# Kernel tuning notes

Measured on AMD Instinct MI355X. Metric: run time of the kernel, lower is better.

The kernel has to match this reference:

```python
import jax, jax.numpy as jnp
import numpy as np

POS_THR = 0.5      # ROI_POSITIVE_THR
NEG_THR = 0.1      # ROI_NEGATIVE_THR
N_SAMPLES = 256    # ROI_SAMPLES
FG_RATIO = 0.25    # ROI_SAMPLE_RATIO
L1W = 1.0          # RPN.L1WEIGHT_INTERSECTION
NUM_FG = int(N_SAMPLES * FG_RATIO)


def _make_boxes(kxy, kwh, shape):
    # valid [x1,y1,x2,y2] boxes in an ~800px image
    xy = jax.random.uniform(kxy, shape[:-1] + (2,)) * 800.0
    wh = jax.random.uniform(kwh, shape[:-1] + (2,)) * 200.0 + 1.0
    return jnp.concatenate([xy, xy + wh], axis=-1)


def setup_inputs() -> dict:
    key = jax.random.key(0)
    k1, k2, k3, k4 = jax.random.split(key, 4)
    proposals = _make_boxes(k1, k2, (16, 16384, 4))  # [B, N, 4]
    gt_boxes = _make_boxes(k3, k4, (16, 128, 4))     # [B, G, 4]
    return {"proposals": proposals, "gt_boxes": gt_boxes}


def _centrehw(b):
    # [x1,y1,x2,y2] -> [cx,cy,w,h]
    x1, y1, x2, y2 = b[..., 0], b[..., 1], b[..., 2], b[..., 3]
    return jnp.stack([(x1 + x2) * 0.5, (y1 + y2) * 0.5, x2 - x1, y2 - y1], axis=-1)


def _targets(gt_c, roi_c):
    dx = (gt_c[..., 0] - roi_c[..., 0]) / roi_c[..., 2]
    dy = (gt_c[..., 1] - roi_c[..., 1]) / roi_c[..., 3]
    dw = jnp.log(gt_c[..., 2] / roi_c[..., 2])
    dh = jnp.log(gt_c[..., 3] / roi_c[..., 3])
    return jnp.stack([dx, dy, dw, dh], axis=-1)


def _iou(prop, gt):
    # prop [B,N,4], gt [B,G,4] -> IoU [B,N,G]
    p = prop[:, :, None, :]
    g = gt[:, None, :, :]
    ix1 = jnp.maximum(p[..., 0], g[..., 0])
    iy1 = jnp.maximum(p[..., 1], g[..., 1])
    ix2 = jnp.minimum(p[..., 2], g[..., 2])
    iy2 = jnp.minimum(p[..., 3], g[..., 3])
    inter = jnp.clip(ix2 - ix1, 0.0) * jnp.clip(iy2 - iy1, 0.0)
    ap = (p[..., 2] - p[..., 0]) * (p[..., 3] - p[..., 1])
    ag = (g[..., 2] - g[..., 0]) * (g[..., 3] - g[..., 1])
    return inter / jnp.maximum(ap + ag - inter, 1e-8)


def _forward(proposals, gt_boxes):
    B, N, _ = proposals.shape
    iou = _iou(proposals, gt_boxes)                       # [B,N,G]
    max_iou = iou.max(axis=-1)                            # [B,N]
    argmax_gt = iou.argmax(axis=-1).astype(jnp.int32)     # [B,N]
    # classify: 1=fg, 0=bg, -1=ignore
    labels = jnp.where(max_iou >= POS_THR, 1,
                       jnp.where(max_iou < NEG_THR, 0, -1)).astype(jnp.int32)
    # randsample: keep <= NUM_FG positives (random), fill rest with negatives.
    r = jax.random.uniform(jax.random.key(1), (B, N))
    pos = labels == 1
    r_pos = jnp.where(pos, r, -1.0)
    order = jnp.argsort(-r_pos, axis=1)
    ranks = jnp.argsort(order, axis=1)                    # rank among positives by r
    pos_sel = pos & (ranks < NUM_FG)
    prio = jnp.where(pos_sel, 3.0 + r,
                     jnp.where(labels == 0, 2.0 + r,
                               jnp.where(pos, 1.0 + r, r)))
    _, idx = jax.lax.top_k(prio, N_SAMPLES)               # [B,S] sampled proposal ids
    batch_labels = jnp.maximum(jnp.take_along_axis(labels, idx, axis=1), 0)  # [B,S]
    roi_batch = jnp.take_along_axis(proposals, idx[..., None], axis=1)       # [B,S,4]
    sel_gt = jnp.take_along_axis(argmax_gt, idx, axis=1)                     # [B,S]
    gt_batch = jnp.take_along_axis(gt_boxes, sel_gt[..., None], axis=1)      # [B,S,4]
    bbox_targets = _targets(_centrehw(gt_batch), _centrehw(roi_batch))       # [B,S,4]
    in_w = jnp.where((batch_labels == 1)[..., None], L1W, 0.0)
    in_w = jnp.broadcast_to(in_w, bbox_targets.shape)
    out_w = (in_w > 0).astype(jnp.float32)
    return roi_batch, batch_labels, bbox_targets, in_w, out_w


def reference(proposals, gt_boxes):
    return _forward(proposals, gt_boxes)
```

## Files before the change

kernel.cpp:

```cpp
#include <hip/hip_runtime.h>
#include <stdint.h>

#define BATCH 16
#define NPROP 16384
#define NGT   128
#define NSAMP 256
#define NFG   64
#define GCAP  512
#define LCAP  8192
#define CSTR  32

typedef unsigned long long ull;

__device__ __forceinline__ void thr_block(uint32_t c0, uint32_t c1,
                                          uint32_t* o0, uint32_t* o1) {
    const uint32_t k0 = 0u, k1 = 1u, ks2 = 0x1BD11BDBu;
    uint32_t x0 = c0 + k0, x1 = c1 + k1;
#define RND(d) { x0 += x1; x1 = (x1 << d) | (x1 >> (32 - d)); x1 ^= x0; }
    RND(13) RND(15) RND(26) RND(6)   x0 += k1;  x1 += ks2 + 1u;
    RND(17) RND(29) RND(16) RND(24)  x0 += ks2; x1 += k0 + 2u;
    RND(13) RND(15) RND(26) RND(6)   x0 += k0;  x1 += k1 + 3u;
    RND(17) RND(29) RND(16) RND(24)  x0 += k1;  x1 += ks2 + 4u;
    RND(13) RND(15) RND(26) RND(6)   x0 += ks2; x1 += k0 + 5u;
#undef RND
    *o0 = x0; *o1 = x1;
}

__device__ __forceinline__ uint32_t thr_part_xor(uint32_t f) {
    uint32_t a, b; thr_block(0u, f, &a, &b);
    return a ^ b;
}

__global__ void k_zero(uint32_t* c) {
    if (threadIdx.x < BATCH * CSTR) c[threadIdx.x] = 0u;
}

__global__ void __launch_bounds__(256) k_compute(
    const float* __restrict__ props, const float* __restrict__ gts,
    ull* __restrict__ lists, uint32_t* __restrict__ cnts)
{
#pragma clang fp contract(off)
    const int b = blockIdx.y;
    const int tid = threadIdx.x;
    const int half = tid & 1;
    const int n = blockIdx.x * 128 + (tid >> 1);
    __shared__ float2 sA[130];
    __shared__ float2 sB[130];
    __shared__ float  sag[130];
    __shared__ uint32_t wcF[4], wcB[4], wcP[4];
    __shared__ uint32_t sEF[4], sEB[4], sBaseF, sBaseB;
    if (tid < NGT) {
        float4 g = ((const float4*)gts)[(size_t)b * NGT + tid];
        int idx = (tid < 64) ? tid : tid + 1;
        sA[idx] = make_float2(g.x, g.y);
        sB[idx] = make_float2(g.z, g.w);
        sag[idx] = (g.z - g.x) * (g.w - g.y);
    }
    __syncthreads();
    const float4 pb = ((const float4*)props)[(size_t)b * NPROP + n];
    const float ap = (pb.z - pb.x) * (pb.w - pb.y);
    float best = -1.0f; int bg = 0;
    const int base  = half ? 65 : 0;
    const int gbias = half ? 64 : 0;
    #pragma unroll 4
    for (int i = 0; i < 64; ++i) {
        const float2 a = sA[base + i];
        const float2 c = sB[base + i];
        float w  = fmaxf(fminf(pb.z, c.x) - fmaxf(pb.x, a.x), 0.0f);
        float hh = fmaxf(fminf(pb.w, c.y) - fmaxf(pb.y, a.y), 0.0f);
        float inter = w * hh;
        float un = fmaxf(ap + sag[base + i] - inter, 1e-8f);
        float iou = inter / un;
        if (iou > best) { best = iou; bg = gbias + i; }
    }
    float ob = __shfl_xor(best, 1);
    int  obg = __shfl_xor(bg, 1);
    if (half == 0 && ob > best) { best = ob; bg = obg; }

    uint32_t lab = (best >= 0.5f) ? 2u : ((best < 0.1f) ? 1u : 0u);
    const uint32_t f = (uint32_t)b * NPROP + (uint32_t)n;
    uint32_t mant = thr_part_xor(f) >> 9;
    ull entry = ((ull)(lab == 2u) << 44) | ((ull)mant << 21)
              | ((ull)(16383u - (uint32_t)n) << 7) | (ull)(uint32_t)bg;

    const bool isEven = (half == 0);
    bool front = isEven && (lab != 0u);
    bool back  = isEven && (lab == 0u);
    bool ispos = isEven && (lab == 2u);
    ull mF = __ballot(front), mB = __ballot(back), mP = __ballot(ispos);
    const int w = tid >> 6;
    const uint32_t lane = (uint32_t)tid & 63u;
    if (lane == 0) {
        wcF[w] = (uint32_t)__popcll(mF);
        wcB[w] = (uint32_t)__popcll(mB);
        wcP[w] = (uint32_t)__popcll(mP);
    }
    __syncthreads();
    if (tid == 0) {
        uint32_t eF = 0, eB = 0, tP = 0;
        #pragma unroll
        for (int i = 0; i < 4; i++) {
            sEF[i] = eF; eF += wcF[i];
            sEB[i] = eB; eB += wcB[i];
            tP += wcP[i];
        }
        sBaseF = eF ? atomicAdd(&cnts[b * CSTR + 0], eF) : 0u;
        sBaseB = eB ? atomicAdd(&cnts[b * CSTR + 1], eB) : 0u;
        if (tP) atomicAdd(&cnts[b * CSTR + 2], tP);
    }
    __syncthreads();
    ull lt = lane ? (~0ull >> (64u - lane)) : 0ull;
    ull* Lb = lists + (size_t)b * NPROP;
    if (front) Lb[sBaseF + sEF[w] + (uint32_t)__popcll(mF & lt)] = entry;
    if (back)  Lb[16383u - (sBaseB + sEB[w] + (uint32_t)__popcll(mB & lt))] = entry;
}

__global__ void __launch_bounds__(1024) k_select(
    const float* __restrict__ props, const float* __restrict__ gts,
    const ull* __restrict__ lists, const uint32_t* __restrict__ cnts,
    float* __restrict__ out)
{
#pragma clang fp contract(off)
    const int b = blockIdx.x;
    const int tid = threadIdx.x;
    __shared__ ull      sf[LCAP];
    __shared__ uint32_t hist[2048];
    __shared__ ull      gat[GCAP];
    __shared__ ull      selk[NSAMP];
    __shared__ uint32_t sela[NSAMP];
    __shared__ uint32_t sh_dig, sh_k, sh_cnt_in, gcnt, selc;
    __shared__ ull sh_thr;

    const ull* Lb = lists + (size_t)b * NPROP;
    const uint32_t npn  = cnts[b * CSTR + 0];
    const uint32_t nig  = cnts[b * CSTR + 1];
    const uint32_t npos = cnts[b * CSTR + 2];
    const bool inLDS = (npn <= LCAP);
    if (inLDS) for (uint32_t j = tid; j < npn; j += 1024) sf[j] = Lb[j];
    if (tid == 0) selc = 0;
    __syncthreads();

    auto getF = [&](uint32_t j) -> ull { return inLDS ? sf[j] : Lb[j]; };
    auto keyA_of = [&](ull e) -> ull {
        return (((e >> 21) & 0x7FFFFFull) << 14) | ((e >> 7) & 0x3FFFull);
    };

    auto locate = [&](uint32_t k) {
        if (tid < 64) {
            const uint32_t lane = (uint32_t)tid;
            uint32_t cs = 0;
            if (lane < 32) {
                const uint32_t base = lane * 64u;
                #pragma unroll 8
                for (uint32_t i = 0; i < 64; i++) cs += hist[base + i];
            }
            uint32_t s = cs;
            #pragma unroll
            for (int off = 1; off < 32; off <<= 1) {
                uint32_t t = __shfl_down(s, off);
                if (lane + off < 32) s += t;
            }
            uint32_t sExcl = s - cs;
            bool cond = (lane < 32) && (sExcl < k) && (k <= s);
            ull ball = __ballot(cond);
            uint32_t cstar = (uint32_t)(__ffsll((unsigned long long)ball) - 1);
            uint32_t kc = (uint32_t)__shfl((int)(k - sExcl), (int)cstar);
            uint32_t val = hist[cstar * 64u + lane];
            uint32_t fi = val;
            #pragma unroll
            for (int off = 1; off < 64; off <<= 1) {
                uint32_t t = __shfl_down(fi, off);
                if (lane + off < 64) fi += t;
            }
            uint32_t fExcl = fi - val;
            bool cond2 = (fExcl < kc) && (kc <= fi);
            ull ball2 = __ballot(cond2);
            uint32_t bstar = (uint32_t)(__ffsll((unsigned long long)ball2) - 1);
            if (lane == bstar) {
                sh_dig = cstar * 64u + lane;
                sh_k = kc - fExcl;
                sh_cnt_in = val;
            }
        }
    };

    auto radix = [&](auto&& kf, uint32_t m, uint32_t k, int shift) -> ull {
        ull prefix = 0, mask = 0;
        for (;;) {
            hist[tid] = 0; hist[tid + 1024] = 0;
            __syncthreads();
            for (uint32_t j = tid; j < m; j += 1024) {
                bool e; ull key = kf(j, e);
                if (e && ((key ^ prefix) & mask) == 0)
                    atomicAdd(&hist[(uint32_t)(key >> shift) & 2047u], 1u);
            }
            __syncthreads();
            locate(k);
            __syncthreads();
            uint32_t dig = sh_dig, kk = sh_k, cnt = sh_cnt_in;
            prefix |= ((ull)dig) << shift;
            mask   |= 2047ull << shift;
            if (cnt <= GCAP || shift == 0) {
                if (tid == 0) gcnt = 0;
                __syncthreads();
                for (uint32_t j = tid; j < m; j += 1024) {
                    bool e; ull key = kf(j, e);
                    if (e && ((key ^ prefix) & mask) == 0) {
                        uint32_t s = atomicAdd(&gcnt, 1u);
                        if (s < GCAP) gat[s] = key;
                    }
                }
                __syncthreads();
                uint32_t gc = (gcnt < GCAP) ? gcnt : GCAP;
                if (tid < (int)gc) {
                    ull x = gat[tid];
                    uint32_t r = 0;
                    for (uint32_t j = 0; j < gc; j++) r += (gat[j] > x);
                    if (r == kk - 1) sh_thr = x;
                }
                __syncthreads();
                return sh_thr;
            } else {
                k = kk;
                shift = (shift >= 11) ? shift - 11 : 0;
                __syncthreads();
            }
        }
    };

    ull thrA = 0;
    if (npos > NFG) {
        thrA = radix([&](uint32_t j, bool& e) -> ull {
            ull ent = getF(j);
            e = ((ent >> 44) & 1ull) != 0;
            return keyA_of(ent);
        }, npn, NFG, 26);
    }

    auto keyB_of = [&](ull ent) -> ull {
        uint32_t mant = (uint32_t)((ent >> 21) & 0x7FFFFFull);
        uint32_t invn = (uint32_t)((ent >> 7) & 0x3FFFull);
        float r = __uint_as_float(0x3F800000u | mant) - 1.0f;
        uint32_t cls;
        if ((ent >> 44) & 1ull) cls = (keyA_of(ent) >= thrA) ? 3u : 1u;
        else cls = 2u;
        float prio = (float)cls + r;
        return (((ull)__float_as_uint(prio)) << 14) | (ull)invn;
    };
    auto key0_of = [&](ull ent) -> ull {
        uint32_t mant = (uint32_t)((ent >> 21) & 0x7FFFFFull);
        uint32_t invn = (uint32_t)((ent >> 7) & 0x3FFFull);
        float r = __uint_as_float(0x3F800000u | mant) - 1.0f;
        float prio = 0.0f + r;
        return (((ull)__float_as_uint(prio)) << 14) | (ull)invn;
    };

    ull thrB = 0, thr0 = 0;
    uint32_t needIgn = 0;
    if (npn >= NSAMP) {
        thrB = radix([&](uint32_t j, bool& e) -> ull { e = true; return keyB_of(getF(j)); },
                     npn, NSAMP, 34);
    } else {
        needIgn = NSAMP - npn;
        thr0 = radix([&](uint32_t j, bool& e) -> ull { e = true; return key0_of(Lb[16383u - j]); },
                     nig, needIgn, 34);
    }
    __syncthreads();

    for (uint32_t j = tid; j < npn; j += 1024) {
        ull ent = getF(j);
        ull key = keyB_of(ent);
        if (npn < NSAMP || key >= thrB) {
            uint32_t s = atomicAdd(&selc, 1u);
            if (s < NSAMP) {
                selk[s] = key;
                sela[s] = ((uint32_t)((ent >> 44) & 1ull) << 7) | (uint32_t)(ent & 0x7Full);
            }
        }
    }
    if (needIgn) {
        for (uint32_t j = tid; j < nig; j += 1024) {
            ull ent = Lb[16383u - j];
            ull key = key0_of(ent);
            if (key >= thr0) {
                uint32_t s = atomicAdd(&selc, 1u);
                if (s < NSAMP) {
                    selk[s] = key;
                    sela[s] = (uint32_t)(ent & 0x7Full);
                }
            }
        }
    }
    __syncthreads();

    if (tid < NSAMP) {
        ull x = selk[tid];
        uint32_t r = 0;
        for (int j = 0; j < NSAMP; j++) r += (selk[j] > x);
        uint32_t n = 16383u - (uint32_t)(x & 0x3FFFull);
        uint32_t aux = sela[tid];
        uint32_t bg = aux & 0x7Fu;
        const int isfg = (int)((aux >> 7) & 1u);
        const float4 pb = ((const float4*)props)[(size_t)b * NPROP + n];
        const float4 gb = ((const float4*)gts)[(size_t)b * NGT + bg];
        const size_t O_ROI = 0;
        const size_t O_LBL = (size_t)BATCH * NSAMP * 4;
        const size_t O_TGT = O_LBL + (size_t)BATCH * NSAMP;
        const size_t O_INW = O_TGT + (size_t)BATCH * NSAMP * 4;
        const size_t O_OUW = O_INW + (size_t)BATCH * NSAMP * 4;
        const size_t row = (size_t)b * NSAMP + r;
        out[O_ROI + row * 4 + 0] = pb.x;
        out[O_ROI + row * 4 + 1] = pb.y;
        out[O_ROI + row * 4 + 2] = pb.z;
        out[O_ROI + row * 4 + 3] = pb.w;
        out[O_LBL + row] = isfg ? 1.0f : 0.0f;
        float rw  = pb.z - pb.x, rh = pb.w - pb.y;
        float gw  = gb.z - gb.x, gh = gb.w - gb.y;
        out[O_TGT + row * 4 + 0] = ((gb.x + gb.z) * 0.5f - (pb.x + pb.z) * 0.5f) / rw;
        out[O_TGT + row * 4 + 1] = ((gb.y + gb.w) * 0.5f - (pb.y + pb.w) * 0.5f) / rh;
        out[O_TGT + row * 4 + 2] = logf(gw / rw);
        out[O_TGT + row * 4 + 3] = logf(gh / rh);
        float wv = isfg ? 1.0f : 0.0f;
        for (int c = 0; c < 4; c++) {
            out[O_INW + row * 4 + c] = wv;
            out[O_OUW + row * 4 + c] = wv;
        }
    }
}

extern "C" void kernel_launch(void* const* d_in, const int* in_sizes, int n_in,
                              void* d_out, int out_size, void* d_ws, size_t ws_size,
                              hipStream_t stream) {
    (void)in_sizes; (void)n_in; (void)out_size; (void)ws_size;
    const float* props = (const float*)d_in[0];
    const float* gts   = (const float*)d_in[1];
    ull* lists = (ull*)d_ws;
    uint32_t* cnts = (uint32_t*)((char*)d_ws + (size_t)BATCH * NPROP * 8);
    float* out = (float*)d_out;

    k_zero<<<1, BATCH * CSTR, 0, stream>>>(cnts);
    dim3 gridA(NPROP / 128, BATCH);
    k_compute<<<gridA, 256, 0, stream>>>(props, gts, lists, cnts);
    k_select<<<BATCH, 1024, 0, stream>>>(props, gts, lists, cnts, out);
}
```

Before: 103.7 us.

## Bucket proposals into pos/high-neg/low-neg/ignore lists to shrink select radix work

The compute kernel now writes each proposal into one of four per-batch lists: positives, negatives with high random mantissa, negatives with low mantissa, and ignored. The select kernel uses the per-bucket counts to work out which priority class holds the cutoff and runs the radix threshold search only over that bucket, often just the high-negative list. Small lists go through a direct rank-count path instead of histogram passes. Counters are padded to separate cache lines. The costs are four times the workspace, an extra ballot and atomic per block, and reliance on the NEGT split putting enough negatives in the high bucket.

After: 96.23 us. 1.08x faster.

```diff
diff --git a/kernel.cpp b/kernel.cpp
--- a/kernel.cpp
+++ b/kernel.cpp
@@ -7,8 +7,8 @@
 #define NSAMP 256
 #define NFG   64
 #define GCAP  512
-#define LCAP  8192
-#define CSTR  32
+#define CSTR  128
+#define NEGT  0x780002u
 
 typedef unsigned long long ull;
 
@@ -32,7 +32,7 @@
 }
 
 __global__ void k_zero(uint32_t* c) {
-    if (threadIdx.x < BATCH * CSTR) c[threadIdx.x] = 0u;
+    for (int i = threadIdx.x; i < BATCH * CSTR; i += 1024) c[i] = 0u;
 }
 
 __global__ void __launch_bounds__(256) k_compute(
@@ -47,8 +47,9 @@
     __shared__ float2 sA[130];
     __shared__ float2 sB[130];
     __shared__ float  sag[130];
-    __shared__ uint32_t wcF[4], wcB[4], wcP[4];
-    __shared__ uint32_t sEF[4], sEB[4], sBaseF, sBaseB;
+    __shared__ uint32_t wc[4][4];
+    __shared__ uint32_t we[4][4];
+    __shared__ uint32_t sBase[4];
     if (tid < NGT) {
         float4 g = ((const float4*)gts)[(size_t)b * NGT + tid];
         int idx = (tid < 64) ? tid : tid + 1;
@@ -84,35 +85,33 @@
               | ((ull)(16383u - (uint32_t)n) << 7) | (ull)(uint32_t)bg;
 
     const bool isEven = (half == 0);
-    bool front = isEven && (lab != 0u);
-    bool back  = isEven && (lab == 0u);
-    bool ispos = isEven && (lab == 2u);
-    ull mF = __ballot(front), mB = __ballot(back), mP = __ballot(ispos);
+    bool cP = isEven && (lab == 2u);
+    bool cH = isEven && (lab == 1u) && (mant >= NEGT);
+    bool cL = isEven && (lab == 1u) && (mant <  NEGT);
+    bool cI = isEven && (lab == 0u);
+    ull mP = __ballot(cP), mH = __ballot(cH), mL = __ballot(cL), mI = __ballot(cI);
     const int w = tid >> 6;
     const uint32_t lane = (uint32_t)tid & 63u;
     if (lane == 0) {
-        wcF[w] = (uint32_t)__popcll(mF);
-        wcB[w] = (uint32_t)__popcll(mB);
-        wcP[w] = (uint32_t)__popcll(mP);
-    }
-    __syncthreads();
-    if (tid == 0) {
-        uint32_t eF = 0, eB = 0, tP = 0;
+        wc[0][w] = (uint32_t)__popcll(mP);
+        wc[1][w] = (uint32_t)__popcll(mH);
+        wc[2][w] = (uint32_t)__popcll(mL);
+        wc[3][w] = (uint32_t)__popcll(mI);
+    }
+    __syncthreads();
+    if (tid < 4) {
+        uint32_t e = 0;
         #pragma unroll
-        for (int i = 0; i < 4; i++) {
-            sEF[i] = eF; eF += wcF[i];
-            sEB[i] = eB; eB += wcB[i];
-            tP += wcP[i];
-        }
-        sBaseF = eF ? atomicAdd(&cnts[b * CSTR + 0], eF) : 0u;
-        sBaseB = eB ? atomicAdd(&cnts[b * CSTR + 1], eB) : 0u;
-        if (tP) atomicAdd(&cnts[b * CSTR + 2], tP);
+        for (int i = 0; i < 4; i++) { we[tid][i] = e; e += wc[tid][i]; }
+        sBase[tid] = e ? atomicAdd(&cnts[b * CSTR + tid * 32], e) : 0u;
     }
     __syncthreads();
     ull lt = lane ? (~0ull >> (64u - lane)) : 0ull;
-    ull* Lb = lists + (size_t)b * NPROP;
-    if (front) Lb[sBaseF + sEF[w] + (uint32_t)__popcll(mF & lt)] = entry;
-    if (back)  Lb[16383u - (sBaseB + sEB[w] + (uint32_t)__popcll(mB & lt))] = entry;
+    ull* slab = lists + ((size_t)b * 4) * NPROP;
+    if (cP) slab[0 * NPROP + sBase[0] + we[0][w] + (uint32_t)__popcll(mP & lt)] = entry;
+    if (cH) slab[1 * NPROP + sBase[1] + we[1][w] + (uint32_t)__popcll(mH & lt)] = entry;
+    if (cL) slab[2 * NPROP + sBase[2] + we[2][w] + (uint32_t)__popcll(mL & lt)] = entry;
+    if (cI) slab[3 * NPROP + sBase[3] + we[3][w] + (uint32_t)__popcll(mI & lt)] = entry;
 }
 
 __global__ void __launch_bounds__(1024) k_select(
@@ -123,7 +122,6 @@
 #pragma clang fp contract(off)
     const int b = blockIdx.x;
     const int tid = threadIdx.x;
-    __shared__ ull      sf[LCAP];
     __shared__ uint32_t hist[2048];
     __shared__ ull      gat[GCAP];
     __shared__ ull      selk[NSAMP];
@@ -131,17 +129,20 @@
     __shared__ uint32_t sh_dig, sh_k, sh_cnt_in, gcnt, selc;
     __shared__ ull sh_thr;
 
-    const ull* Lb = lists + (size_t)b * NPROP;
-    const uint32_t npn  = cnts[b * CSTR + 0];
-    const uint32_t nig  = cnts[b * CSTR + 1];
-    const uint32_t npos = cnts[b * CSTR + 2];
-    const bool inLDS = (npn <= LCAP);
-    if (inLDS) for (uint32_t j = tid; j < npn; j += 1024) sf[j] = Lb[j];
+    const ull* Ppos  = lists + ((size_t)b * 4 + 0) * NPROP;
+    const ull* PnegH = lists + ((size_t)b * 4 + 1) * NPROP;
+    const ull* PnegL = lists + ((size_t)b * 4 + 2) * NPROP;
+    const ull* Pign  = lists + ((size_t)b * 4 + 3) * NPROP;
+    const uint32_t npos = cnts[b * CSTR + 0];
+    const uint32_t nH   = cnts[b * CSTR + 32];
+    const uint32_t nL   = cnts[b * CSTR + 64];
+    const uint32_t nig  = cnts[b * CSTR + 96];
+    const uint32_t nneg = nH + nL;
+    const uint32_t npn  = npos + nneg;
     if (tid == 0) selc = 0;
     __syncthreads();
 
-    auto getF = [&](uint32_t j) -> ull { return inLDS ? sf[j] : Lb[j]; };
-    auto keyA_of = [&](ull e) -> ull {
+    auto keyA_of = [](ull e) -> ull {
         return (((e >> 21) & 0x7FFFFFull) << 14) | ((e >> 7) & 0x3FFFull);
     };
 
@@ -185,6 +186,24 @@
     };
 
     auto radix = [&](auto&& kf, uint32_t m, uint32_t k, int shift) -> ull {
+        if (m <= GCAP) {
+            if (tid == 0) gcnt = 0;
+            __syncthreads();
+            for (uint32_t j = tid; j < m; j += 1024) {
+                bool e; ull key = kf(j, e);
+                if (e) { uint32_t s = atomicAdd(&gcnt, 1u); gat[s] = key; }
+            }
+            __syncthreads();
+            uint32_t gc = gcnt;
+            if (tid < (int)gc) {
+                ull x = gat[tid];
+                uint32_t r = 0;
+                for (uint32_t j = 0; j < gc; j++) r += (gat[j] > x);
+                if (r == k - 1) sh_thr = x;
+            }
+            __syncthreads();
+            return sh_thr;
+        }
         ull prefix = 0, mask = 0;
         for (;;) {
             hist[tid] = 0; hist[tid + 1024] = 0;
@@ -231,23 +250,25 @@
     ull thrA = 0;
     if (npos > NFG) {
         thrA = radix([&](uint32_t j, bool& e) -> ull {
-            ull ent = getF(j);
-            e = ((ent >> 44) & 1ull) != 0;
-            return keyA_of(ent);
-        }, npn, NFG, 26);
-    }
-
-    auto keyB_of = [&](ull ent) -> ull {
+            e = true; return keyA_of(Ppos[j]); }, npos, NFG, 26);
+    }
+
+    auto keyB_pos = [&](ull ent) -> ull {
         uint32_t mant = (uint32_t)((ent >> 21) & 0x7FFFFFull);
         uint32_t invn = (uint32_t)((ent >> 7) & 0x3FFFull);
         float r = __uint_as_float(0x3F800000u | mant) - 1.0f;
-        uint32_t cls;
-        if ((ent >> 44) & 1ull) cls = (keyA_of(ent) >= thrA) ? 3u : 1u;
-        else cls = 2u;
+        uint32_t cls = (keyA_of(ent) >= thrA) ? 3u : 1u;
         float prio = (float)cls + r;
         return (((ull)__float_as_uint(prio)) << 14) | (ull)invn;
     };
-    auto key0_of = [&](ull ent) -> ull {
+    auto keyB_neg = [](ull ent) -> ull {
+        uint32_t mant = (uint32_t)((ent >> 21) & 0x7FFFFFull);
+        uint32_t invn = (uint32_t)((ent >> 7) & 0x3FFFull);
+        float r = __uint_as_float(0x3F800000u | mant) - 1.0f;
+        float prio = 2.0f + r;
+        return (((ull)__float_as_uint(prio)) << 14) | (ull)invn;
+    };
+    auto keyB_ign = [](ull ent) -> ull {
         uint32_t mant = (uint32_t)((ent >> 21) & 0x7FFFFFull);
         uint32_t invn = (uint32_t)((ent >> 7) & 0x3FFFull);
         float r = __uint_as_float(0x3F800000u | mant) - 1.0f;
@@ -255,40 +276,58 @@
         return (((ull)__float_as_uint(prio)) << 14) | (ull)invn;
     };
 
-    ull thrB = 0, thr0 = 0;
-    uint32_t needIgn = 0;
-    if (npn >= NSAMP) {
-        thrB = radix([&](uint32_t j, bool& e) -> ull { e = true; return keyB_of(getF(j)); },
-                     npn, NSAMP, 34);
+    const uint32_t c3 = (npos < NFG) ? npos : NFG;
+    const uint32_t c2 = nneg;
+    uint32_t clsStar = (npn >= NSAMP) ? ((NSAMP <= c3 + c2) ? 2u : 1u) : 0u;
+    bool scanL = true;
+    const bool scanI = (clsStar == 0u);
+    ull thrB = 0;
+    if (clsStar == 2u) {
+        uint32_t k2 = NSAMP - c3;
+        if (nH >= k2) {
+            scanL = false;
+            thrB = radix([&](uint32_t j, bool& e) -> ull {
+                e = true; return keyB_neg(PnegH[j]); }, nH, k2, 25);
+        } else {
+            thrB = radix([&](uint32_t j, bool& e) -> ull {
+                e = true; return keyB_neg(j < nH ? PnegH[j] : PnegL[j - nH]); },
+                nneg, k2, 25);
+        }
+    } else if (clsStar == 1u) {
+        uint32_t k1 = NSAMP - c3 - c2;
+        thrB = radix([&](uint32_t j, bool& e) -> ull {
+            ull kb = keyB_pos(Ppos[j]);
+            e = ((kb >> 14) < 0x40000000ull);
+            return kb; }, npos, k1, 26);
     } else {
-        needIgn = NSAMP - npn;
-        thr0 = radix([&](uint32_t j, bool& e) -> ull { e = true; return key0_of(Lb[16383u - j]); },
-                     nig, needIgn, 34);
-    }
-    __syncthreads();
-
-    for (uint32_t j = tid; j < npn; j += 1024) {
-        ull ent = getF(j);
-        ull key = keyB_of(ent);
-        if (npn < NSAMP || key >= thrB) {
-            uint32_t s = atomicAdd(&selc, 1u);
-            if (s < NSAMP) {
-                selk[s] = key;
-                sela[s] = ((uint32_t)((ent >> 44) & 1ull) << 7) | (uint32_t)(ent & 0x7Full);
-            }
-        }
-    }
-    if (needIgn) {
+        uint32_t k0 = NSAMP - npn;
+        thrB = radix([&](uint32_t j, bool& e) -> ull {
+            e = true; return keyB_ign(Pign[j]); }, nig, k0, 34);
+    }
+    __syncthreads();
+
+    auto push = [&](ull key, ull ent, uint32_t fg) {
+        uint32_t s = atomicAdd(&selc, 1u);
+        if (s < NSAMP) { selk[s] = key; sela[s] = (fg << 7) | (uint32_t)(ent & 0x7Full); }
+    };
+    for (uint32_t j = tid; j < npos; j += 1024) {
+        ull ent = Ppos[j]; ull key = keyB_pos(ent);
+        if (clsStar == 0u || key >= thrB) push(key, ent, 1u);
+    }
+    for (uint32_t j = tid; j < nH; j += 1024) {
+        ull ent = PnegH[j]; ull key = keyB_neg(ent);
+        if (clsStar == 0u || key >= thrB) push(key, ent, 0u);
+    }
+    if (scanL) {
+        for (uint32_t j = tid; j < nL; j += 1024) {
+            ull ent = PnegL[j]; ull key = keyB_neg(ent);
+            if (clsStar == 0u || key >= thrB) push(key, ent, 0u);
+        }
+    }
+    if (scanI) {
         for (uint32_t j = tid; j < nig; j += 1024) {
-            ull ent = Lb[16383u - j];
-            ull key = key0_of(ent);
-            if (key >= thr0) {
-                uint32_t s = atomicAdd(&selc, 1u);
-                if (s < NSAMP) {
-                    selk[s] = key;
-                    sela[s] = (uint32_t)(ent & 0x7Full);
-                }
-            }
+            ull ent = Pign[j]; ull key = keyB_ign(ent);
+            if (key >= thrB) push(key, ent, 0u);
         }
     }
     __syncthreads();
@@ -297,7 +336,7 @@
         ull x = selk[tid];
         uint32_t r = 0;
         for (int j = 0; j < NSAMP; j++) r += (selk[j] > x);
-        uint32_t n = 16383u - (uint32_t)(x & 0x3FFFull);
+        uint32_t n = 16383u - (uint32_t)((x >> 0) & 0x3FFFull);
         uint32_t aux = sela[tid];
         uint32_t bg = aux & 0x7Fu;
         const int isfg = (int)((aux >> 7) & 1u);
@@ -335,10 +374,10 @@
     const float* props = (const float*)d_in[0];
     const float* gts   = (const float*)d_in[1];
     ull* lists = (ull*)d_ws;
-    uint32_t* cnts = (uint32_t*)((char*)d_ws + (size_t)BATCH * NPROP * 8);
+    uint32_t* cnts = (uint32_t*)((char*)d_ws + (size_t)BATCH * 4 * NPROP * 8);
     float* out = (float*)d_out;
 
-    k_zero<<<1, BATCH * CSTR, 0, stream>>>(cnts);
+    k_zero<<<1, 1024, 0, stream>>>(cnts);
     dim3 gridA(NPROP / 128, BATCH);
     k_compute<<<gridA, 256, 0, stream>>>(props, gts, lists, cnts);
     k_select<<<BATCH, 1024, 0, stream>>>(props, gts, lists, cnts, out);
```
